# Kernel tuning notes

Hardware: AMD Instinct MI355X
Metric: run time of the kernel (lower is better)

Reference implementation:

```python
import jax, jax.numpy as jnp
import numpy as np


def setup_inputs() -> dict:
    key = jax.random.key(0)
    k1, k2, k3, k4 = jax.random.split(key, 4)
    B, H_in, W_in = 512, 128, 64
    H_out, W_out, K = 256, 64, 4
    x = jax.random.normal(k1, (B, H_in, W_in), dtype=jnp.float32)
    mask = jax.random.randint(k2, (H_out, K), 0, H_in, dtype=jnp.int64)
    # stacked per-group weights (width_out, width_in*K) and biases (width_out,)
    W = jax.random.normal(k3, (H_out, W_out, W_in * K), dtype=jnp.float32) * 0.05
    b = jax.random.normal(k4, (H_out, W_out), dtype=jnp.float32) * 0.05
    return {"x": x, "mask": mask, "W": W, "b": b}


def reference(x, mask, W, b):
    # x: [B, H_in, W_in]; mask: [H_out, K]; W: [H_out, W_out, K*W_in]; b: [H_out, W_out]
    B = x.shape[0]
    H_out, K = mask.shape
    # gather rows per group: [B, H_out, K, W_in]
    gathered = x[:, mask, :]
    # flatten kernel window: [B, H_out, K*W_in]
    gathered = gathered.reshape(B, H_out, -1)
    # per-group linear: out[b,h,o] = sum_d gathered[b,h,d] * W[h,o,d] + b[h,o]
    out = jnp.einsum('bhd,hod->bho', gathered, W) + b[None, :, :]
    return out  # [B, H_out, W_out]
```

## Files before the change

kernel.cpp:

```cpp
#include <hip/hip_runtime.h>

constexpr int H_OUT = 256;
constexpr int D     = 256;

typedef __bf16 bf16x8 __attribute__((ext_vector_type(8)));
typedef float  f32x16 __attribute__((ext_vector_type(16)));

__device__ inline ushort f2bf(float f) {
    uint u = __float_as_uint(f);
    u = (u + 0x7FFFu + ((u >> 16) & 1u)) >> 16;
    return (ushort)u;
}

__device__ inline uint2 pack4(float4 v) {
    uint2 r;
    r.x = (uint)f2bf(v.x) | ((uint)f2bf(v.y) << 16);
    r.y = (uint)f2bf(v.z) | ((uint)f2bf(v.w) << 16);
    return r;
}

__global__ __launch_bounds__(256, 2) void sparse_linear_mfma3(
    const float* __restrict__ x,
    const int*   __restrict__ mask,
    const float* __restrict__ W,
    const float* __restrict__ bias,
    float*       __restrict__ out)
{
    const int bx   = blockIdx.x;
    const int h    = bx & 255;
    const int half = bx >> 8;
    const int tid  = threadIdx.x;
    const int lane = tid & 63, wid = tid >> 6;
    const int wr   = (wid >> 1) * 32;
    const int wc   = (wid & 1) * 32;
    const int rowl = lane & 31, hi = lane >> 5;

    __shared__ float4 Wls[64 * 32];
    __shared__ float4 Xls[64 * 32];

    {
        const int wrow = tid >> 6;
        const int c    = tid & 63;
        const float4* wsrc = (const float4*)(W + (size_t)h * 64 * D);
        #pragma unroll
        for (int p = 0; p < 16; ++p) {
            const int R = p * 4 + wrow;
            const float4 v = wsrc[R * 64 + c];
            const int s = c >> 1, hf = c & 1;
            *((uint2*)&Wls[R * 32 + (s ^ (R & 15))] + hf) = pack4(v);
        }
    }

    const int xrr = tid >> 4;
    const int xc  = tid & 15;
    int mq[4];
    #pragma unroll
    for (int q = 0; q < 4; ++q) mq[q] = mask[h * 4 + q];

    float4 xr[16];

    #pragma unroll
    for (int p = 0; p < 16; ++p) {
        const int q  = p >> 2;
        const int rr = (p & 3) * 16 + xrr;
        xr[p] = *(const float4*)(x + ((size_t)(half * 256 + rr) * 128 + mq[q]) * 64 + xc * 4);
    }
    #pragma unroll
    for (int p = 0; p < 16; ++p) {
        const int q  = p >> 2;
        const int rr = (p & 3) * 16 + xrr;
        const int s  = q * 8 + (xc >> 1), hf = xc & 1;
        *((uint2*)&Xls[rr * 32 + (s ^ (rr & 15))] + hf) = pack4(xr[p]);
    }
    __syncthreads();

    const int   ra = wr + rowl;
    const int   rb = wc + rowl;
    const float bv = bias[h * 64 + wc + rowl];

    #pragma unroll
    for (int bt = 0; bt < 4; ++bt) {
        if (bt < 3) {
            #pragma unroll
            for (int p = 0; p < 16; ++p) {
                const int q  = p >> 2;
                const int rr = (p & 3) * 16 + xrr;
                xr[p] = *(const float4*)(x + ((size_t)(half * 256 + (bt + 1) * 64 + rr) * 128
                                              + mq[q]) * 64 + xc * 4);
            }
        }

        f32x16 acc0 = {}, acc1 = {};
        #pragma unroll
        for (int ks = 0; ks < 16; ks += 2) {
            bf16x8 a0 = __builtin_bit_cast(bf16x8, Xls[ra * 32 + ((ks * 2 + hi) ^ (ra & 15))]);
            bf16x8 b0 = __builtin_bit_cast(bf16x8, Wls[rb * 32 + ((ks * 2 + hi) ^ (rb & 15))]);
            bf16x8 a1 = __builtin_bit_cast(bf16x8, Xls[ra * 32 + (((ks + 1) * 2 + hi) ^ (ra & 15))]);
            bf16x8 b1 = __builtin_bit_cast(bf16x8, Wls[rb * 32 + (((ks + 1) * 2 + hi) ^ (rb & 15))]);
            acc0 = __builtin_amdgcn_mfma_f32_32x32x16_bf16(a0, b0, acc0, 0, 0, 0);
            acc1 = __builtin_amdgcn_mfma_f32_32x32x16_bf16(a1, b1, acc1, 0, 0, 0);
        }

        #pragma unroll
        for (int reg = 0; reg < 16; ++reg) {
            const int rl = (reg & 3) + 8 * (reg >> 2) + 4 * hi;
            const size_t b = (size_t)half * 256 + bt * 64 + wr + rl;
            out[(b * H_OUT + h) * 64 + wc + rowl] = acc0[reg] + acc1[reg] + bv;
        }

        if (bt < 3) {
            __syncthreads();
            #pragma unroll
            for (int p = 0; p < 16; ++p) {
                const int q  = p >> 2;
                const int rr = (p & 3) * 16 + xrr;
                const int s  = q * 8 + (xc >> 1), hf = xc & 1;
                *((uint2*)&Xls[rr * 32 + (s ^ (rr & 15))] + hf) = pack4(xr[p]);
            }
            __syncthreads();
        }
    }
}

extern "C" void kernel_launch(void* const* d_in, const int* in_sizes, int n_in,
                              void* d_out, int out_size, void* d_ws, size_t ws_size,
                              hipStream_t stream) {
    const float* x    = (const float*)d_in[0];
    const int*   mask = (const int*)d_in[1];
    const float* W    = (const float*)d_in[2];
    const float* bias = (const float*)d_in[3];
    float* out = (float*)d_out;

    dim3 grid(512);
    dim3 block(256);
    sparse_linear_mfma3<<<grid, block, 0, stream>>>(x, mask, W, bias, out);
}
```

Baseline: 97.52 us.

## Load gathered x straight into MFMA fragments and split batch across more blocks

The X shared-memory staging is removed. Each lane now loads its gathered x rows directly from global memory into registers, converts them to bf16 fragments in place, and prefetches two k-steps ahead. The grid doubles so each block covers 128 batch rows of one group, with block indices interleaved across groups. Occupancy is raised to 4 blocks per CU now that less shared memory is used. The intent is to drop the LDS round trip and the barriers around it, at the cost of more uncoalesced 32-byte global loads and W being loaded twice as often.

```diff
diff --git a/kernel.cpp b/kernel.cpp
--- a/kernel.cpp
+++ b/kernel.cpp
@@ -6,20 +6,25 @@
 typedef __bf16 bf16x8 __attribute__((ext_vector_type(8)));
 typedef float  f32x16 __attribute__((ext_vector_type(16)));
 
-__device__ inline ushort f2bf(float f) {
+__device__ __forceinline__ ushort f2bf(float f) {
     uint u = __float_as_uint(f);
     u = (u + 0x7FFFu + ((u >> 16) & 1u)) >> 16;
     return (ushort)u;
 }
-
-__device__ inline uint2 pack4(float4 v) {
-    uint2 r;
-    r.x = (uint)f2bf(v.x) | ((uint)f2bf(v.y) << 16);
-    r.y = (uint)f2bf(v.z) | ((uint)f2bf(v.w) << 16);
-    return r;
+__device__ __forceinline__ uint pack2(float a, float b) {
+    return (uint)f2bf(a) | ((uint)f2bf(b) << 16);
+}
+__device__ __forceinline__ uint2 pack4(float4 v) {
+    uint2 r; r.x = pack2(v.x, v.y); r.y = pack2(v.z, v.w); return r;
+}
+__device__ __forceinline__ bf16x8 packfrag(float4 lo, float4 hi4) {
+    uint4 o;
+    o.x = pack2(lo.x, lo.y);  o.y = pack2(lo.z, lo.w);
+    o.z = pack2(hi4.x, hi4.y); o.w = pack2(hi4.z, hi4.w);
+    return __builtin_bit_cast(bf16x8, o);
 }
 
-__global__ __launch_bounds__(256, 2) void sparse_linear_mfma3(
+__global__ __launch_bounds__(256, 4) void sparse_linear_v6(
     const float* __restrict__ x,
     const int*   __restrict__ mask,
     const float* __restrict__ W,
@@ -27,98 +32,73 @@
     float*       __restrict__ out)
 {
     const int bx   = blockIdx.x;
-    const int h    = bx & 255;
-    const int half = bx >> 8;
+    const int h    = ((bx >> 5) << 3) | (bx & 7);
+    const int bq   = (bx >> 3) & 3;
     const int tid  = threadIdx.x;
     const int lane = tid & 63, wid = tid >> 6;
-    const int wr   = (wid >> 1) * 32;
-    const int wc   = (wid & 1) * 32;
     const int rowl = lane & 31, hi = lane >> 5;
 
     __shared__ float4 Wls[64 * 32];
-    __shared__ float4 Xls[64 * 32];
+
+    int mq[4];
+    #pragma unroll
+    for (int q = 0; q < 4; ++q) mq[q] = mask[h * 4 + q];
+
+    const float* xb = x + (size_t)(bq * 128 + wid * 32 + rowl) * (128 * 64);
+
+    float4 pa0, pb0, pa1, pb1;
+    {
+        const int k00 = hi * 8;
+        const float* p0 = xb + mq[0] * 64 + k00;
+        pa0 = ((const float4*)p0)[0]; pb0 = ((const float4*)p0)[1];
+        const int k01 = 16 + hi * 8;
+        const float* p1 = xb + mq[0] * 64 + k01;
+        pa1 = ((const float4*)p1)[0]; pb1 = ((const float4*)p1)[1];
+    }
 
     {
+        const int c    = tid & 63;
         const int wrow = tid >> 6;
-        const int c    = tid & 63;
         const float4* wsrc = (const float4*)(W + (size_t)h * 64 * D);
         #pragma unroll
         for (int p = 0; p < 16; ++p) {
             const int R = p * 4 + wrow;
-            const float4 v = wsrc[R * 64 + c];
-            const int s = c >> 1, hf = c & 1;
-            *((uint2*)&Wls[R * 32 + (s ^ (R & 15))] + hf) = pack4(v);
+            const float4 v = wsrc[(size_t)R * 64 + c];
+            *((uint2*)&Wls[R * 32 + ((c >> 1) ^ (R & 15))] + (c & 1)) = pack4(v);
         }
-    }
-
-    const int xrr = tid >> 4;
-    const int xc  = tid & 15;
-    int mq[4];
-    #pragma unroll
-    for (int q = 0; q < 4; ++q) mq[q] = mask[h * 4 + q];
-
-    float4 xr[16];
-
-    #pragma unroll
-    for (int p = 0; p < 16; ++p) {
-        const int q  = p >> 2;
-        const int rr = (p & 3) * 16 + xrr;
-        xr[p] = *(const float4*)(x + ((size_t)(half * 256 + rr) * 128 + mq[q]) * 64 + xc * 4);
-    }
-    #pragma unroll
-    for (int p = 0; p < 16; ++p) {
-        const int q  = p >> 2;
-        const int rr = (p & 3) * 16 + xrr;
-        const int s  = q * 8 + (xc >> 1), hf = xc & 1;
-        *((uint2*)&Xls[rr * 32 + (s ^ (rr & 15))] + hf) = pack4(xr[p]);
     }
     __syncthreads();
 
-    const int   ra = wr + rowl;
-    const int   rb = wc + rowl;
-    const float bv = bias[h * 64 + wc + rowl];
+    const int xv = rowl & 15;
+    f32x16 acc0 = {}, acc1 = {};
 
     #pragma unroll
-    for (int bt = 0; bt < 4; ++bt) {
-        if (bt < 3) {
-            #pragma unroll
-            for (int p = 0; p < 16; ++p) {
-                const int q  = p >> 2;
-                const int rr = (p & 3) * 16 + xrr;
-                xr[p] = *(const float4*)(x + ((size_t)(half * 256 + (bt + 1) * 64 + rr) * 128
-                                              + mq[q]) * 64 + xc * 4);
-            }
+    for (int ks = 0; ks < 16; ++ks) {
+        const bf16x8 a = (ks & 1) ? packfrag(pa1, pb1) : packfrag(pa0, pb0);
+
+        if (ks + 2 < 16) {
+            const int kn = (ks + 2) * 16 + hi * 8;
+            const float* pn = xb + mq[kn >> 6] * 64 + (kn & 63);
+            if (ks & 1) { pa1 = ((const float4*)pn)[0]; pb1 = ((const float4*)pn)[1]; }
+            else        { pa0 = ((const float4*)pn)[0]; pb0 = ((const float4*)pn)[1]; }
         }
 
-        f32x16 acc0 = {}, acc1 = {};
-        #pragma unroll
-        for (int ks = 0; ks < 16; ks += 2) {
-            bf16x8 a0 = __builtin_bit_cast(bf16x8, Xls[ra * 32 + ((ks * 2 + hi) ^ (ra & 15))]);
-            bf16x8 b0 = __builtin_bit_cast(bf16x8, Wls[rb * 32 + ((ks * 2 + hi) ^ (rb & 15))]);
-            bf16x8 a1 = __builtin_bit_cast(bf16x8, Xls[ra * 32 + (((ks + 1) * 2 + hi) ^ (ra & 15))]);
-            bf16x8 b1 = __builtin_bit_cast(bf16x8, Wls[rb * 32 + (((ks + 1) * 2 + hi) ^ (rb & 15))]);
-            acc0 = __builtin_amdgcn_mfma_f32_32x32x16_bf16(a0, b0, acc0, 0, 0, 0);
-            acc1 = __builtin_amdgcn_mfma_f32_32x32x16_bf16(a1, b1, acc1, 0, 0, 0);
-        }
+        const int s = ks * 2 + hi;
+        const bf16x8 b0 = __builtin_bit_cast(bf16x8, Wls[rowl * 32 + (s ^ xv)]);
+        const bf16x8 b1 = __builtin_bit_cast(bf16x8, Wls[(32 + rowl) * 32 + (s ^ xv)]);
+        acc0 = __builtin_amdgcn_mfma_f32_32x32x16_bf16(a, b0, acc0, 0, 0, 0);
+        acc1 = __builtin_amdgcn_mfma_f32_32x32x16_bf16(a, b1, acc1, 0, 0, 0);
+    }
 
-        #pragma unroll
-        for (int reg = 0; reg < 16; ++reg) {
-            const int rl = (reg & 3) + 8 * (reg >> 2) + 4 * hi;
-            const size_t b = (size_t)half * 256 + bt * 64 + wr + rl;
-            out[(b * H_OUT + h) * 64 + wc + rowl] = acc0[reg] + acc1[reg] + bv;
-        }
-
-        if (bt < 3) {
-            __syncthreads();
-            #pragma unroll
-            for (int p = 0; p < 16; ++p) {
-                const int q  = p >> 2;
-                const int rr = (p & 3) * 16 + xrr;
-                const int s  = q * 8 + (xc >> 1), hf = xc & 1;
-                *((uint2*)&Xls[rr * 32 + (s ^ (rr & 15))] + hf) = pack4(xr[p]);
-            }
-            __syncthreads();
-        }
+    const float bv0 = bias[h * 64 + rowl];
+    const float bv1 = bias[h * 64 + 32 + rowl];
+    #pragma unroll
+    for (int reg = 0; reg < 16; ++reg) {
+        const int rl = (reg & 3) + 8 * (reg >> 2) + 4 * hi;
+        const size_t b = (size_t)bq * 128 + wid * 32 + rl;
+        float* o = out + (b * H_OUT + h) * 64;
+        o[rowl]      = acc0[reg] + bv0;
+        o[32 + rowl] = acc1[reg] + bv1;
     }
 }
 
@@ -131,7 +111,7 @@
     const float* bias = (const float*)d_in[3];
     float* out = (float*)d_out;
 
-    dim3 grid(512);
+    dim3 grid(1024);
     dim3 block(256);
-    sparse_linear_mfma3<<<grid, block, 0, stream>>>(x, mask, W, bias, out);
+    sparse_linear_v6<<<grid, block, 0, stream>>>(x, mask, W, bias, out);
 }
```

After: 104.1 us. 1.07x slower.
